# Performance work log

Hardware: AMD Instinct MI355X
Metric: run time of the kernel (lower is better)

## Reference

```python
import jax, jax.numpy as jnp
import numpy as np

NNZ_A = 1_048_576   # nonzeros (tuple entries) in A, each with D features
NNZ_B = 1_048_576   # nonzeros in adjacency B (scalar values)
M = 4_194_304       # intermediate multiplication events (acd coordinate list)
TAR_NNZ = 1_048_576 # nonzeros in the output sparse tensor
D = 64              # feature channels


def setup_inputs() -> dict:
    key = jax.random.key(0)
    k1, k2, k3, k4, k5 = jax.random.split(key, 5)
    Aval = jax.random.normal(k1, (NNZ_A, D), dtype=jnp.float32)
    Bval = jax.random.normal(k2, (NNZ_B,), dtype=jnp.float32)
    # Precomputed coordinate descriptor: for each multiplication event m,
    # acd0[m] = output nonzero index, acd1[m] = index into Aval, acd2[m] = index into Bval.
    acd0 = jnp.sort(jax.random.randint(k3, (M,), 0, TAR_NNZ, dtype=jnp.int64))
    acd1 = jax.random.randint(k4, (M,), 0, NNZ_A, dtype=jnp.int64)
    acd2 = jax.random.randint(k5, (M,), 0, NNZ_B, dtype=jnp.int64)
    return {"Aval": Aval, "Bval": Bval, "acd0": acd0, "acd1": acd1,
            "acd2": acd2, "tar_nnz": TAR_NNZ}


def reference(Aval, Bval, acd0, acd1, acd2, tar_nnz):
    # spspmm with cached acd descriptor, aggr='sum':
    #   mult[m, :] = Aval[acd1[m], :] * Bval[acd2[m]]
    #   out[t, :]  = sum_{m: acd0[m]==t} mult[m, :]
    mult = Aval[acd1] * Bval[acd2][:, None]            # [M, D]
    out = jax.ops.segment_sum(mult, acd0, num_segments=tar_nnz)  # [tar_nnz, D]
    return out
```

## Files before the change

kernel.cpp:

```cpp
#include <hip/hip_runtime.h>

typedef float f4 __attribute__((ext_vector_type(4)));

#define EV_G 64
#define NG   4
#define EPW  (EV_G * NG)
#define WPB  4

__global__ __launch_bounds__(256) void prezero_kernel(
    const int* __restrict__ acd0, float* __restrict__ out, int ngroups, int M)
{
    const int task = blockIdx.x * 16 + (threadIdx.x >> 4);
    const int s    = threadIdx.x & 15;
    if (task >= 2 * ngroups) return;
    long m = (long)(task >> 1) * EV_G + ((task & 1) ? (EV_G - 1) : 0);
    if (m >= M) m = M - 1;
    const int t = acd0[m];
    f4 z = {0.f, 0.f, 0.f, 0.f};
    __builtin_nontemporal_store(z, (f4*)(out + (size_t)t * 64 + s * 4));
}

__global__ __launch_bounds__(256, 4) void spspmm_seg_kernel(
    const float* __restrict__ Aval,
    const float* __restrict__ Bval,
    const int*   __restrict__ acd0,
    const int*   __restrict__ acd1,
    const int*   __restrict__ acd2,
    float*       __restrict__ out,
    int M, int TAR)
{
    const int lane = threadIdx.x & 63;
    const int s    = lane & 15;
    const int g    = lane >> 4;
    const int wid  = blockIdx.x * WPB + (threadIdx.x >> 6);
    const long gm0 = (long)wid * EPW + (long)g * EV_G;
    if (gm0 >= M) return;
    const long gEnd = (gm0 + EV_G < (long)M) ? gm0 + EV_G : (long)M;
    const int  nev  = (int)(gEnd - gm0);

    const f4 z4 = {0.f, 0.f, 0.f, 0.f};

    const int t_first = acd0[gm0];
    const int t_prev  = (gm0 > 0) ? acd0[gm0 - 1] : -1;
    for (int t = t_prev + 1; t < t_first; ++t)
        __builtin_nontemporal_store(z4, (f4*)(out + (size_t)t * 64 + s * 4));

    f4  acc   = z4;
    int cur_t = t_first;

    auto flush = [&](int next_t) {
        float* p = out + (size_t)cur_t * 64 + s * 4;
        if (cur_t == t_first) {
            atomicAdd(p + 0, acc[0]); atomicAdd(p + 1, acc[1]);
            atomicAdd(p + 2, acc[2]); atomicAdd(p + 3, acc[3]);
        } else {
            __builtin_nontemporal_store(acc, (f4*)p);
        }
        for (int tz = cur_t + 1; tz < next_t; ++tz)
            __builtin_nontemporal_store(z4, (f4*)(out + (size_t)tz * 64 + s * 4));
        acc   = z4;
        cur_t = next_t;
    };

    if (nev == EV_G) {
        #pragma unroll 1
        for (int c = 0; c < EV_G / 16; ++c) {
            const long mb = gm0 + c * 16;
            const int   t_i = __builtin_nontemporal_load(acd0 + mb + s);
            const int   a_i = __builtin_nontemporal_load(acd1 + mb + s);
            const float b_i = Bval[__builtin_nontemporal_load(acd2 + mb + s)];
            f4 v[16];
            #pragma unroll
            for (int j = 0; j < 16; ++j) {
                const int a = __shfl(a_i, j, 16);
                v[j] = *(const f4*)(Aval + (size_t)a * 64 + s * 4);
            }
            #pragma unroll
            for (int j = 0; j < 16; ++j) {
                const int   t  = __shfl(t_i, j, 16);
                const float bv = __shfl(b_i, j, 16);
                if (t != cur_t) flush(t);
                acc += v[j] * bv;
            }
        }
    } else {
        for (int m = 0; m < nev; ++m) {
            const int   t  = acd0[gm0 + m];
            const int   a  = acd1[gm0 + m];
            const float bv = Bval[acd2[gm0 + m]];
            const f4    v  = *(const f4*)(Aval + (size_t)a * 64 + s * 4);
            if (t != cur_t) flush(t);
            acc += v * bv;
        }
    }

    {
        float* p = out + (size_t)cur_t * 64 + s * 4;
        atomicAdd(p + 0, acc[0]); atomicAdd(p + 1, acc[1]);
        atomicAdd(p + 2, acc[2]); atomicAdd(p + 3, acc[3]);
    }

    if (gEnd == M) {
        const int tl = acd0[M - 1];
        for (int t = tl + 1; t < TAR; ++t)
            __builtin_nontemporal_store(z4, (f4*)(out + (size_t)t * 64 + s * 4));
    }
}

extern "C" void kernel_launch(void* const* d_in, const int* in_sizes, int n_in,
                              void* d_out, int out_size, void* d_ws, size_t ws_size,
                              hipStream_t stream) {
    const float* Aval = (const float*)d_in[0];
    const float* Bval = (const float*)d_in[1];
    const int*   acd0 = (const int*)d_in[2];
    const int*   acd1 = (const int*)d_in[3];
    const int*   acd2 = (const int*)d_in[4];
    float* out = (float*)d_out;
    const int M   = in_sizes[2];
    const int TAR = out_size / 64;

    const int ngroups = (M + EV_G - 1) / EV_G;

    {
        const int tasks  = 2 * ngroups;
        const int blocks = (tasks + 15) / 16;
        prezero_kernel<<<dim3(blocks), dim3(256), 0, stream>>>(acd0, out, ngroups, M);
    }

    const long nwaves = ((long)M + EPW - 1) / EPW;
    const long blocks = (nwaves + WPB - 1) / WPB;
    spspmm_seg_kernel<<<dim3((unsigned)blocks), dim3(WPB * 64), 0, stream>>>(
        Aval, Bval, acd0, acd1, acd2, out, M, TAR);
}
```

Before: 301.7 us.

## Double-buffer A-row gathers across chunks and double events per group

Software-pipelines the segmented gather/accumulate loop with two register buffers, so the descriptor loads and Aval gathers for the next 16-event chunk are issued before the current chunk is scanned. Events per 16-lane group go from 64 to 128, which halves the number of boundary atomics and the prezero work, and the occupancy hint drops from 4 to 3 blocks to make room for the extra registers. The cost is more register pressure and fewer waves resident to hide latency, plus less parallelism because each wave now does twice the work.

```diff
diff --git a/kernel.cpp b/kernel.cpp
--- a/kernel.cpp
+++ b/kernel.cpp
@@ -2,10 +2,12 @@
 
 typedef float f4 __attribute__((ext_vector_type(4)));
 
-#define EV_G 64
+#define EV_G 128
 #define NG   4
 #define EPW  (EV_G * NG)
 #define WPB  4
+#define CH   16
+#define NCH  (EV_G / CH)
 
 __global__ __launch_bounds__(256) void prezero_kernel(
     const int* __restrict__ acd0, float* __restrict__ out, int ngroups, int M)
@@ -20,7 +22,7 @@
     __builtin_nontemporal_store(z, (f4*)(out + (size_t)t * 64 + s * 4));
 }
 
-__global__ __launch_bounds__(256, 4) void spspmm_seg_kernel(
+__global__ __launch_bounds__(256, 3) void spspmm_seg_kernel(
     const float* __restrict__ Aval,
     const float* __restrict__ Bval,
     const int*   __restrict__ acd0,
@@ -62,26 +64,39 @@
         cur_t = next_t;
     };
 
+    auto desc = [&](int c, int &t, int &a, float &b) {
+        const long mb = gm0 + (long)c * CH + s;
+        t = __builtin_nontemporal_load(acd0 + mb);
+        a = __builtin_nontemporal_load(acd1 + mb);
+        b = Bval[__builtin_nontemporal_load(acd2 + mb)];
+    };
+    auto gather = [&](f4 (&v)[CH], int a_i) {
+        #pragma unroll
+        for (int j = 0; j < CH; ++j) {
+            const int a = __shfl(a_i, j, 16);
+            v[j] = *(const f4*)(Aval + (size_t)a * 64 + s * 4);
+        }
+    };
+    auto scan = [&](const f4 (&v)[CH], int t_i, float b_i) {
+        #pragma unroll
+        for (int j = 0; j < CH; ++j) {
+            const int   t  = __shfl(t_i, j, 16);
+            const float bv = __shfl(b_i, j, 16);
+            if (t != cur_t) flush(t);
+            acc += v[j] * bv;
+        }
+    };
+
     if (nev == EV_G) {
+        int tA, aA, tB, aB; float bA, bB;
+        f4 vA[CH], vB[CH];
+        desc(0, tA, aA, bA); gather(vA, aA);
         #pragma unroll 1
-        for (int c = 0; c < EV_G / 16; ++c) {
-            const long mb = gm0 + c * 16;
-            const int   t_i = __builtin_nontemporal_load(acd0 + mb + s);
-            const int   a_i = __builtin_nontemporal_load(acd1 + mb + s);
-            const float b_i = Bval[__builtin_nontemporal_load(acd2 + mb + s)];
-            f4 v[16];
-            #pragma unroll
-            for (int j = 0; j < 16; ++j) {
-                const int a = __shfl(a_i, j, 16);
-                v[j] = *(const f4*)(Aval + (size_t)a * 64 + s * 4);
-            }
-            #pragma unroll
-            for (int j = 0; j < 16; ++j) {
-                const int   t  = __shfl(t_i, j, 16);
-                const float bv = __shfl(b_i, j, 16);
-                if (t != cur_t) flush(t);
-                acc += v[j] * bv;
-            }
+        for (int c = 0; c < NCH; c += 2) {
+            desc(c + 1, tB, aB, bB); gather(vB, aB);
+            scan(vA, tA, bA);
+            if (c + 2 < NCH) { desc(c + 2, tA, aA, bA); gather(vA, aA); }
+            scan(vB, tB, bB);
         }
     } else {
         for (int m = 0; m < nev; ++m) {
```

Result: slower. 324.3 us (+7.5%).

## Gather bf16 copy of Aval and use plain stores for unshared segments

Applied to the files above, without the earlier changes.

Each call first runs a new kernel that converts Aval to a bf16 copy in workspace. The main kernel then gathers 8-byte bf16 rows instead of 16-byte fp32 rows, widening them back to fp32 before accumulating, which halves the bytes of the dominant random gather. Separately, a segment now falls back to atomicAdd only when it truly spans a group boundary. Otherwise it uses a plain store, and the pre-zero kernel only clears rows that are shared across groups. The price is an extra full read-and-write pass over Aval per call and lost precision in A's values, which may exceed the accuracy tolerance.

```diff
diff --git a/kernel.cpp b/kernel.cpp
--- a/kernel.cpp
+++ b/kernel.cpp
@@ -1,27 +1,58 @@
 #include <hip/hip_runtime.h>
 
-typedef float f4 __attribute__((ext_vector_type(4)));
+typedef float          f4    __attribute__((ext_vector_type(4)));
+typedef unsigned short u16x4 __attribute__((ext_vector_type(4)));
 
 #define EV_G 64
 #define NG   4
 #define EPW  (EV_G * NG)
 #define WPB  4
+#define CH   16
+
+__device__ __forceinline__ unsigned short f2bf(float f) {
+    unsigned u = __float_as_uint(f);
+    return (unsigned short)((u + 0x7fffu + ((u >> 16) & 1u)) >> 16);
+}
+__device__ __forceinline__ f4 tofloat(f4 v) { return v; }
+__device__ __forceinline__ f4 tofloat(u16x4 u) {
+    f4 r;
+    r[0] = __uint_as_float((unsigned)u[0] << 16);
+    r[1] = __uint_as_float((unsigned)u[1] << 16);
+    r[2] = __uint_as_float((unsigned)u[2] << 16);
+    r[3] = __uint_as_float((unsigned)u[3] << 16);
+    return r;
+}
+
+__global__ __launch_bounds__(256) void conv_kernel(
+    const float* __restrict__ A, unsigned short* __restrict__ Abf, long n4)
+{
+    long i = (long)blockIdx.x * 256 + threadIdx.x;
+    const long stride = (long)gridDim.x * 256;
+    for (; i < n4; i += stride) {
+        f4 v = __builtin_nontemporal_load(((const f4*)A) + i);
+        u16x4 o;
+        o[0] = f2bf(v[0]); o[1] = f2bf(v[1]); o[2] = f2bf(v[2]); o[3] = f2bf(v[3]);
+        ((u16x4*)Abf)[i] = o;
+    }
+}
 
 __global__ __launch_bounds__(256) void prezero_kernel(
     const int* __restrict__ acd0, float* __restrict__ out, int ngroups, int M)
 {
     const int task = blockIdx.x * 16 + (threadIdx.x >> 4);
     const int s    = threadIdx.x & 15;
-    if (task >= 2 * ngroups) return;
-    long m = (long)(task >> 1) * EV_G + ((task & 1) ? (EV_G - 1) : 0);
-    if (m >= M) m = M - 1;
+    if (task < 1 || task >= ngroups) return;
+    const long m = (long)task * EV_G;
+    if (m >= M) return;
     const int t = acd0[m];
+    if (acd0[m - 1] != t) return;
     f4 z = {0.f, 0.f, 0.f, 0.f};
     __builtin_nontemporal_store(z, (f4*)(out + (size_t)t * 64 + s * 4));
 }
 
+template <typename AT>
 __global__ __launch_bounds__(256, 4) void spspmm_seg_kernel(
-    const float* __restrict__ Aval,
+    const AT*    __restrict__ Aval,
     const float* __restrict__ Bval,
     const int*   __restrict__ acd0,
     const int*   __restrict__ acd1,
@@ -29,6 +60,9 @@
     float*       __restrict__ out,
     int M, int TAR)
 {
+    typedef __attribute__((ext_vector_type(4)))
+        typename std::conditional<sizeof(AT) == 2, unsigned short, float>::type VecT;
+
     const int lane = threadIdx.x & 63;
     const int s    = lane & 15;
     const int g    = lane >> 4;
@@ -41,21 +75,26 @@
     const f4 z4 = {0.f, 0.f, 0.f, 0.f};
 
     const int t_first = acd0[gm0];
-    const int t_prev  = (gm0 > 0) ? acd0[gm0 - 1] : -1;
+    const int t_prev  = (gm0 > 0)   ? acd0[gm0 - 1] : -1;
+    const int t_next  = (gEnd < M)  ? acd0[gEnd]    : -1;
+
     for (int t = t_prev + 1; t < t_first; ++t)
         __builtin_nontemporal_store(z4, (f4*)(out + (size_t)t * 64 + s * 4));
 
     f4  acc   = z4;
     int cur_t = t_first;
 
-    auto flush = [&](int next_t) {
+    auto store_acc = [&](bool shared) {
         float* p = out + (size_t)cur_t * 64 + s * 4;
-        if (cur_t == t_first) {
+        if (shared) {
             atomicAdd(p + 0, acc[0]); atomicAdd(p + 1, acc[1]);
             atomicAdd(p + 2, acc[2]); atomicAdd(p + 3, acc[3]);
         } else {
             __builtin_nontemporal_store(acc, (f4*)p);
         }
+    };
+    auto flush = [&](int next_t) {
+        store_acc(cur_t == t_first && cur_t == t_prev);
         for (int tz = cur_t + 1; tz < next_t; ++tz)
             __builtin_nontemporal_store(z4, (f4*)(out + (size_t)tz * 64 + s * 4));
         acc   = z4;
@@ -64,23 +103,23 @@
 
     if (nev == EV_G) {
         #pragma unroll 1
-        for (int c = 0; c < EV_G / 16; ++c) {
-            const long mb = gm0 + c * 16;
+        for (int c = 0; c < EV_G / CH; ++c) {
+            const long mb = gm0 + (long)c * CH;
             const int   t_i = __builtin_nontemporal_load(acd0 + mb + s);
             const int   a_i = __builtin_nontemporal_load(acd1 + mb + s);
             const float b_i = Bval[__builtin_nontemporal_load(acd2 + mb + s)];
-            f4 v[16];
+            VecT v[CH];
             #pragma unroll
-            for (int j = 0; j < 16; ++j) {
+            for (int j = 0; j < CH; ++j) {
                 const int a = __shfl(a_i, j, 16);
-                v[j] = *(const f4*)(Aval + (size_t)a * 64 + s * 4);
+                v[j] = *(const VecT*)(Aval + (size_t)a * 64 + s * 4);
             }
             #pragma unroll
-            for (int j = 0; j < 16; ++j) {
+            for (int j = 0; j < CH; ++j) {
                 const int   t  = __shfl(t_i, j, 16);
                 const float bv = __shfl(b_i, j, 16);
                 if (t != cur_t) flush(t);
-                acc += v[j] * bv;
+                acc += tofloat(v[j]) * bv;
             }
         }
     } else {
@@ -88,17 +127,13 @@
             const int   t  = acd0[gm0 + m];
             const int   a  = acd1[gm0 + m];
             const float bv = Bval[acd2[gm0 + m]];
-            const f4    v  = *(const f4*)(Aval + (size_t)a * 64 + s * 4);
+            const VecT  v  = *(const VecT*)(Aval + (size_t)a * 64 + s * 4);
             if (t != cur_t) flush(t);
-            acc += v * bv;
+            acc += tofloat(v) * bv;
         }
     }
 
-    {
-        float* p = out + (size_t)cur_t * 64 + s * 4;
-        atomicAdd(p + 0, acc[0]); atomicAdd(p + 1, acc[1]);
-        atomicAdd(p + 2, acc[2]); atomicAdd(p + 3, acc[3]);
-    }
+    store_acc((cur_t == t_next) || (cur_t == t_first && cur_t == t_prev));
 
     if (gEnd == M) {
         const int tl = acd0[M - 1];
@@ -118,17 +153,25 @@
     float* out = (float*)d_out;
     const int M   = in_sizes[2];
     const int TAR = out_size / 64;
+    const long nA_elems = in_sizes[0];
 
     const int ngroups = (M + EV_G - 1) / EV_G;
 
     {
-        const int tasks  = 2 * ngroups;
-        const int blocks = (tasks + 15) / 16;
+        const int blocks = (ngroups + 15) / 16;
         prezero_kernel<<<dim3(blocks), dim3(256), 0, stream>>>(acd0, out, ngroups, M);
     }
 
     const long nwaves = ((long)M + EPW - 1) / EPW;
     const long blocks = (nwaves + WPB - 1) / WPB;
-    spspmm_seg_kernel<<<dim3((unsigned)blocks), dim3(WPB * 64), 0, stream>>>(
-        Aval, Bval, acd0, acd1, acd2, out, M, TAR);
+
+    if (ws_size >= (size_t)nA_elems * 2) {
+        unsigned short* Abf = (unsigned short*)d_ws;
+        conv_kernel<<<dim3(2048), dim3(256), 0, stream>>>(Aval, Abf, nA_elems / 4);
+        spspmm_seg_kernel<unsigned short><<<dim3((unsigned)blocks), dim3(WPB * 64), 0, stream>>>(
+            Abf, Bval, acd0, acd1, acd2, out, M, TAR);
+    } else {
+        spspmm_seg_kernel<float><<<dim3((unsigned)blocks), dim3(WPB * 64), 0, stream>>>(
+            Aval, Bval, acd0, acd1, acd2, out, M, TAR);
+    }
 }
```

Measured after the change: 280.2 us. 1.08x faster.
